# Kernel optimization log

Measured on AMD Instinct MI355X. Metric: run time of the kernel, lower is better.

The kernel has to match this reference:

```python
import jax, jax.numpy as jnp
import numpy as np

B, L, D, H, P, NL, TOPK = 2, 512, 512, 16, 128, 2, 3
DH = D // H
FF = 4 * D
EPS = 1e-5
NEG = -1e9


def _ln(h):
    mu = jnp.mean(h, axis=-1, keepdims=True)
    var = jnp.mean((h - mu) ** 2, axis=-1, keepdims=True)
    return (h - mu) * jax.lax.rsqrt(var + EPS)


def setup_inputs() -> dict:
    key = jax.random.key(0)
    ks = jax.random.split(key, 16)
    def nrm(k, shape, s=0.02):
        return jax.random.normal(k, shape, dtype=jnp.float32) * s
    lengths = jax.random.randint(ks[0], (B,), L // 2, L + 1)
    padding_mask = jnp.arange(L)[None, :] >= lengths[:, None]  # [B,L] bool, True = pad
    return {
        'x': jax.random.normal(ks[1], (L, B, D), dtype=jnp.float32),
        'pos': jax.random.normal(ks[2], (B, L, 3), dtype=jnp.float32),
        'time_emb': jax.random.normal(ks[3], (B, 1, D), dtype=jnp.float32),
        'pair_feat': jax.random.normal(ks[4], (B, L, L, P), dtype=jnp.float32),
        'pos_emb_w': nrm(ks[5], (D, 3), 0.1),
        'pfb_w': nrm(ks[6], (H, P), 0.1),
        'p2n_w1': nrm(ks[7], (P, P)),
        'p2n_w2': nrm(ks[8], (D, P)),
        'adaln_w': nrm(ks[9], (NL, 6 * D, D)),
        'adaln_b': jnp.zeros((NL, 6 * D), jnp.float32),
        'qkv_w': nrm(ks[10], (NL, 3 * D, D)),
        'qkv_b': jnp.zeros((NL, 3 * D), jnp.float32),
        'proj_w': nrm(ks[11], (NL, D, D)),
        'proj_b': jnp.zeros((NL, D), jnp.float32),
        'mlp_w1': nrm(ks[12], (NL, FF, D)),
        'mlp_b1': jnp.zeros((NL, FF), jnp.float32),
        'mlp_w2': nrm(ks[13], (NL, D, FF)),
        'mlp_b2': jnp.zeros((NL, D), jnp.float32),
        'padding_mask': padding_mask,
    }


def _forward(x, pos, time_emb, pair_feat, pos_emb_w, pfb_w, p2n_w1, p2n_w2,
             adaln_w, adaln_b, qkv_w, qkv_b, proj_w, proj_b,
             mlp_w1, mlp_b1, mlp_w2, mlp_b2, padding_mask):
    x = jnp.swapaxes(x, 0, 1)  # [B,L,D]
    keep = (~padding_mask).astype(x.dtype)  # [B,L]
    pos_embedding = (pos @ pos_emb_w.T) * keep[..., None]  # [B,L,D], masked_fill(pad,0)
    # pair bias: SiLU -> Linear(P,H), then permute to [B,H,L,L]
    pfb = jnp.einsum('blmp,hp->bhlm', jax.nn.silu(pair_feat), pfb_w)
    # mask pair features on both residue axes
    pf = pair_feat * keep[:, None, :, None] * keep[:, :, None, None]  # [B,L,L,P]
    # topk over dim=1 (rows) per (b, col): transpose so rows are last axis
    col_scores = jnp.swapaxes(jnp.mean(pfb, axis=1), 1, 2)  # [B, L(col), L(row)]
    _, idx = jax.lax.top_k(col_scores, TOPK)  # [B, L, K]
    idx = jnp.moveaxis(idx, 2, 1)  # [B, K, L]
    f2n = jnp.mean(jnp.take_along_axis(pf, idx[..., None], axis=1), axis=1)  # [B,L,P]
    f2n = jax.nn.silu(f2n @ p2n_w1.T) @ p2n_w2.T  # pair2node MLP -> [B,L,D]
    x = x + f2n  # condition stream
    cond = jax.nn.silu(x)
    scale = 1.0 / np.sqrt(DH)
    h = pos_embedding
    for l in range(NL):  # DiT blocks (adaLN modulation from cond, MHA with pair bias, GELU MLP)
        hin = h + time_emb
        mod = cond @ adaln_w[l].T + adaln_b[l]  # [B,L,6D]
        sh_a, sc_a, g_a, sh_m, sc_m, g_m = jnp.split(mod, 6, axis=-1)
        a = _ln(hin) * (1.0 + sc_a) + sh_a
        q, k, v = jnp.split(a @ qkv_w[l].T + qkv_b[l], 3, axis=-1)
        q = q.reshape(B, L, H, DH)
        k = k.reshape(B, L, H, DH)
        v = v.reshape(B, L, H, DH)
        s = jnp.einsum('blhd,bmhd->bhlm', q, k) * scale + pfb
        s = jnp.where(padding_mask[:, None, None, :], NEG, s)
        o = jnp.einsum('bhlm,bmhd->blhd', jax.nn.softmax(s, axis=-1), v).reshape(B, L, D)
        hin = hin + g_a * (o @ proj_w[l].T + proj_b[l])
        m = _ln(hin) * (1.0 + sc_m) + sh_m
        m = jax.nn.gelu(m @ mlp_w1[l].T + mlp_b1[l]) @ mlp_w2[l].T + mlp_b2[l]
        h = hin + g_m * m
    return h  # [B,L,D]


def reference(x, pos, time_emb, pair_feat, pos_emb_w, pfb_w, p2n_w1, p2n_w2,
              adaln_w, adaln_b, qkv_w, qkv_b, proj_w, proj_b,
              mlp_w1, mlp_b1, mlp_w2, mlp_b2, padding_mask):
    return _forward(x, pos, time_emb, pair_feat, pos_emb_w, pfb_w, p2n_w1, p2n_w2,
                    adaln_w, adaln_b, qkv_w, qkv_b, proj_w, proj_b,
                    mlp_w1, mlp_b1, mlp_w2, mlp_b2, padding_mask)
```

## Files before the change

kernel.cpp:

```cpp
#include <hip/hip_runtime.h>
#include <hip/hip_bf16.h>
#include <math.h>

#define B_  2
#define L_  512
#define D_  512
#define H_  16
#define P_  128
#define NL_ 2
#define DH_ 32
#define FF_ 2048
#define NT_ (B_*L_)

typedef __bf16 bf16_t;
typedef bf16_t bf16x8 __attribute__((ext_vector_type(8)));
typedef bf16_t bf16x4 __attribute__((ext_vector_type(4)));
typedef bf16_t bf16x2 __attribute__((ext_vector_type(2)));
typedef float  f32x4  __attribute__((ext_vector_type(4)));

__device__ __forceinline__ float siluf(float x){ return x / (1.f + __expf(-x)); }
__device__ __forceinline__ float geluf(float x){
  const float c = 0.7978845608028654f;
  float x3 = x*x*x;
  return 0.5f*x*(1.f + tanhf(c*(x + 0.044715f*x3)));
}

__device__ __forceinline__ void gload16(const bf16_t* g, bf16_t* l){
  __builtin_amdgcn_global_load_lds(
      (const __attribute__((address_space(1))) unsigned int*)g,
      (__attribute__((address_space(3))) unsigned int*)l, 16, 0, 0);
}

__global__ __launch_bounds__(256) void k_cvtw(const float* __restrict__ s0,
      const float* __restrict__ s1, const float* __restrict__ s2,
      const float* __restrict__ s3, const float* __restrict__ s4,
      bf16_t* __restrict__ dst){
  const size_t c0=3145728, c1=4718592, c2=5242880, c3=7340032, c4=9437184;
  size_t e = ((size_t)blockIdx.x*256 + threadIdx.x)*4;
  if (e >= c4) return;
  const float* s; size_t off;
  if      (e < c0){ s=s0; off=e; }
  else if (e < c1){ s=s1; off=e-c0; }
  else if (e < c2){ s=s2; off=e-c1; }
  else if (e < c3){ s=s3; off=e-c2; }
  else            { s=s4; off=e-c3; }
  float4 v = *(const float4*)(s + off);
  bf16x4 o; o[0]=(bf16_t)v.x; o[1]=(bf16_t)v.y; o[2]=(bf16_t)v.z; o[3]=(bf16_t)v.w;
  *(bf16x4*)(dst + e) = o;
}

__global__ __launch_bounds__(256) void k_posemb(const float* __restrict__ pos,
      const float* __restrict__ w, const int* __restrict__ maskp,
      float* __restrict__ h, float* __restrict__ keepf){
  int n = blockIdx.x;
  float kf = (maskp[n] != 0) ? 0.f : 1.f;
  if (threadIdx.x == 0) keepf[n] = kf;
  float p0 = pos[n*3+0], p1 = pos[n*3+1], p2 = pos[n*3+2];
  for (int d = threadIdx.x; d < D_; d += 256){
    float v = p0*w[d*3+0] + p1*w[d*3+1] + p2*w[d*3+2];
    h[(size_t)n*D_ + d] = kf*v;
  }
}

__global__ __launch_bounds__(256) void k_pfb2(const float* __restrict__ pair,
      const float* __restrict__ w, bf16_t* __restrict__ pfb, float* __restrict__ colm){
  int blk = blockIdx.x;
  int mc = blk & 1;
  int n  = blk >> 1;
  int b = n >> 9, l = n & 511;
  int tid = threadIdx.x;
  __shared__ float sw[16][128];
  {
    float4* swv = (float4*)&sw[0][0];
    const float4* wv = (const float4*)w;
    swv[tid] = wv[tid];
    swv[tid + 256] = wv[tid + 256];
  }
  __syncthreads();
  int m = mc*256 + tid;
  const float* rowp = pair + (((size_t)n)*512 + m)*128;
  float acc[16] = {};
  #pragma unroll 4
  for (int pc = 0; pc < 32; ++pc){
    float4 v = ((const float4*)rowp)[pc];
    v.x = siluf(v.x); v.y = siluf(v.y); v.z = siluf(v.z); v.w = siluf(v.w);
    #pragma unroll
    for (int hh = 0; hh < 16; ++hh){
      float4 wv = *(const float4*)&sw[hh][pc*4];
      acc[hh] += v.x*wv.x + v.y*wv.y + v.z*wv.z + v.w*wv.w;
    }
  }
  float mean = 0.f;
  #pragma unroll
  for (int hh = 0; hh < 16; ++hh) mean += acc[hh];
  colm[((size_t)n)*512 + m] = mean * (1.f/16.f);
  #pragma unroll
  for (int hh = 0; hh < 16; ++hh)
    pfb[(((size_t)(b*16 + hh))*512 + l)*512 + m] = (bf16_t)acc[hh];
}

__global__ __launch_bounds__(128) void k_topk_f2n(const float* __restrict__ colm,
      const float* __restrict__ pair, const float* __restrict__ keepf,
      const float* __restrict__ w1, const float* __restrict__ w2,
      const float* __restrict__ xin, bf16_t* __restrict__ cond){
  int n = blockIdx.x; int b = n >> 9, m = n & 511;
  __shared__ int sidx[3];
  __shared__ float f2n_s[128];
  __shared__ float u_s[128];
  int tid = threadIdx.x;
  if (tid < 64){
    const float* colbase = colm + ((size_t)b*512)*512 + m;
    float v[8];
    #pragma unroll
    for (int i = 0; i < 8; ++i) v[i] = colbase[(size_t)(tid + 64*i)*512];
    int c0 = -1, c1 = -1;
    for (int r = 0; r < 3; ++r){
      float bv = -INFINITY; int bi = 1 << 30;
      #pragma unroll
      for (int i = 0; i < 8; ++i){
        int idx = tid + 64*i;
        bool excl = (idx == c0) || (idx == c1);
        float val = v[i];
        if (!excl && (val > bv || (val == bv && idx < bi))){ bv = val; bi = idx; }
      }
      for (int o = 32; o > 0; o >>= 1){
        float ov = __shfl_down(bv, o);
        int   oi = __shfl_down(bi, o);
        if (ov > bv || (ov == bv && oi < bi)){ bv = ov; bi = oi; }
      }
      bi = __shfl(bi, 0);
      if (tid == 0) sidx[r] = bi;
      if (r == 0) c0 = bi; else c1 = bi;
    }
  }
  __syncthreads();
  int i0 = sidx[0], i1 = sidx[1], i2 = sidx[2];
  float kc = keepf[n];
  float k0 = keepf[b*512 + i0], k1 = keepf[b*512 + i1], k2 = keepf[b*512 + i2];
  {
    int p = tid;
    float s = k0*pair[(((size_t)(b*512 + i0))*512 + m)*128 + p]
            + k1*pair[(((size_t)(b*512 + i1))*512 + m)*128 + p]
            + k2*pair[(((size_t)(b*512 + i2))*512 + m)*128 + p];
    f2n_s[p] = s * kc * (1.f/3.f);
  }
  __syncthreads();
  {
    int j = tid;
    const float* wr = w1 + (size_t)j*128;
    float acc = 0.f;
    #pragma unroll 8
    for (int p = 0; p < 128; ++p) acc += f2n_s[p]*wr[p];
    u_s[j] = siluf(acc);
  }
  __syncthreads();
  for (int d = tid; d < 512; d += 128){
    const float* wr = w2 + (size_t)d*128;
    float acc = 0.f;
    #pragma unroll 8
    for (int p = 0; p < 128; ++p) acc += u_s[p]*wr[p];
    float xv = xin[((size_t)(m*2 + b))*512 + d];
    cond[(size_t)n*512 + d] = (bf16_t)siluf(xv + acc);
  }
}

__global__ __launch_bounds__(128) void k_lnmod2(const float* __restrict__ hbase,
      const float* __restrict__ te, const float* __restrict__ mod,
      bf16_t* __restrict__ out, int sh_off, int sc_off){
  int n = blockIdx.x; int b = n >> 9;
  int tid = threadIdx.x;
  float4 v = ((const float4*)(hbase + (size_t)n*512))[tid];
  if (te){
    float4 t = ((const float4*)(te + (size_t)b*512))[tid];
    v.x += t.x; v.y += t.y; v.z += t.z; v.w += t.w;
  }
  float s = v.x + v.y + v.z + v.w;
  float q = v.x*v.x + v.y*v.y + v.z*v.z + v.w*v.w;
  #pragma unroll
  for (int o = 1; o < 64; o <<= 1){ s += __shfl_xor(s, o); q += __shfl_xor(q, o); }
  __shared__ float s2[2], q2[2];
  if ((tid & 63) == 0){ s2[tid >> 6] = s; q2[tid >> 6] = q; }
  __syncthreads();
  float S = s2[0] + s2[1], Q = q2[0] + q2[1];
  float mean = S * (1.f/512.f);
  float var  = Q * (1.f/512.f) - mean*mean;
  float rstd = rsqrtf(var + 1e-5f);
  const float* mrow = mod + (size_t)n*3072;
  float4 sc = *(const float4*)(mrow + sc_off + tid*4);
  float4 sh = *(const float4*)(mrow + sh_off + tid*4);
  bf16x4 rv;
  rv[0] = (bf16_t)((v.x - mean)*rstd*(1.f + sc.x) + sh.x);
  rv[1] = (bf16_t)((v.y - mean)*rstd*(1.f + sc.y) + sh.y);
  rv[2] = (bf16_t)((v.z - mean)*rstd*(1.f + sc.z) + sh.z);
  rv[3] = (bf16_t)((v.w - mean)*rstd*(1.f + sc.w) + sh.w);
  *(bf16x4*)(out + (size_t)n*512 + tid*4) = rv;
}

template<bool SMALL>
__global__ __launch_bounds__(256) void k_gemm_bf(const bf16_t* __restrict__ A,
      const bf16_t* __restrict__ Bw, const float* __restrict__ bias,
      int M, int N, int K, int epi,
      float* __restrict__ outf, bf16_t* __restrict__ outb,
      const float* __restrict__ res, const float* __restrict__ gate,
      const float* __restrict__ te, bf16_t* __restrict__ vT){
  const int BN = SMALL ? 32 : 64;
  __shared__ __align__(16) bf16_t As[64*64];
  __shared__ __align__(16) bf16_t Bs[(SMALL?32:64)*64];
  int tid = threadIdx.x;
  int m0 = blockIdx.y*64, n0 = blockIdx.x*BN;
  int lane = tid & 63, wid = tid >> 6;
  int wr = SMALL ? wid : (wid>>1);
  int wc = SMALL ? 0 : (wid&1);
  const int FM = SMALL ? 1 : 2;
  const int WMR = SMALL ? 16 : 32;
  int frow = lane & 15, g = lane >> 4;
  f32x4 acc[2][2] = {};
  for (int k0 = 0; k0 < K; k0 += 64){
    {
      int e = tid;
      #pragma unroll
      for (int i = 0; i < 2; ++i, e += 256){
        int row = e >> 3, cb = e & 7;
        gload16(A + (size_t)(m0+row)*K + k0 + ((cb ^ (row&7))<<3), As + e*8);
      }
      e = tid;
      #pragma unroll
      for (int i = 0; i < (SMALL?1:2); ++i, e += 256){
        int row = e >> 3, cb = e & 7;
        gload16(Bw + (size_t)(n0+row)*K + k0 + ((cb ^ (row&7))<<3), Bs + e*8);
      }
    }
    __syncthreads();
    #pragma unroll
    for (int ks = 0; ks < 2; ++ks){
      bf16x8 af[2], bfv[2];
      #pragma unroll
      for (int fm = 0; fm < FM; ++fm){
        int ar = wr*WMR + fm*16 + frow;
        af[fm] = *(const bf16x8*)&As[ar*64 + (((ks*4+g) ^ (ar&7))<<3)];
      }
      #pragma unroll
      for (int fn = 0; fn < 2; ++fn){
        int br = wc*32 + fn*16 + frow;
        bfv[fn] = *(const bf16x8*)&Bs[br*64 + (((ks*4+g) ^ (br&7))<<3)];
      }
      #pragma unroll
      for (int fm = 0; fm < FM; ++fm)
        #pragma unroll
        for (int fn = 0; fn < 2; ++fn)
          acc[fm][fn] = __builtin_amdgcn_mfma_f32_16x16x32_bf16(af[fm], bfv[fn], acc[fm][fn], 0,0,0);
    }
    __syncthreads();
  }
  #pragma unroll
  for (int fm = 0; fm < FM; ++fm){
    #pragma unroll
    for (int fn = 0; fn < 2; ++fn){
      int n = n0 + wc*32 + fn*16 + frow;
      float bb = bias[n];
      int row0 = m0 + wr*WMR + fm*16 + g*4;
      if (epi == 3 && n >= 1024){
        int hh = (n-1024)>>5, dh = (n-1024)&31;
        int b = row0>>9, ll = row0&511;
        bf16x4 pv;
        #pragma unroll
        for (int i = 0; i < 4; ++i){
          float v = acc[fm][fn][i] + bb;
          outb[(size_t)(row0+i)*N + n] = (bf16_t)v;
          pv[i] = (bf16_t)v;
        }
        *(bf16x4*)&vT[(((size_t)(b*16+hh))*32 + dh)*512 + ll] = pv;
      } else {
        #pragma unroll
        for (int i = 0; i < 4; ++i){
          int row = row0 + i;
          float v = acc[fm][fn][i] + bb;
          if (epi == 1){
            v = res[(size_t)row*N + n] + te[(row>>9)*D_ + n] + gate[(size_t)row*(6*D_) + n]*v;
            outf[(size_t)row*N + n] = v;
          } else if (epi == 2){
            outb[(size_t)row*N + n] = (bf16_t)geluf(v);
          } else if (epi == 3){
            outb[(size_t)row*N + n] = (bf16_t)v;
          } else if (epi == 4){
            v = res[(size_t)row*N + n] + gate[(size_t)row*(6*D_) + n]*v;
            outf[(size_t)row*N + n] = v;
          } else {
            outf[(size_t)row*N + n] = v;
          }
        }
      }
    }
  }
}

__global__ __launch_bounds__(256) void k_attn2(const bf16_t* __restrict__ qkv,
      const bf16_t* __restrict__ vT, const bf16_t* __restrict__ pfb,
      const float* __restrict__ keepf, bf16_t* __restrict__ obuf){
  __shared__ float ss[16][516];
  __shared__ float opart[4][16][33];
  __shared__ float inv_s[16];
  int blk = blockIdx.x;
  int qt = blk & 31;
  int bh = blk >> 5;
  int b = bh >> 4, h = bh & 15;
  int r0 = qt*16;
  int tid = threadIdx.x;
  int lane = tid & 63, w = tid >> 6;
  int frow = lane & 15, g = lane >> 4;
  const float scale = 0.17677669529663687f;
  bf16x8 qf = *(const bf16x8*)(qkv + (size_t)(b*512 + r0 + frow)*1536 + h*32 + g*8);
  for (int t = 0; t < 8; ++t){
    int kc = w*128 + t*16;
    bf16x8 kf = *(const bf16x8*)(qkv + (size_t)(b*512 + kc + frow)*1536 + 512 + h*32 + g*8);
    f32x4 s4 = {};
    s4 = __builtin_amdgcn_mfma_f32_16x16x32_bf16(qf, kf, s4, 0,0,0);
    int tok = kc + frow;
    float kp = keepf[b*512 + tok];
    const bf16_t* pf = pfb + ((size_t)bh*512 + r0 + g*4)*512 + tok;
    #pragma unroll
    for (int i = 0; i < 4; ++i){
      float sv = s4[i]*scale + (float)pf[(size_t)i*512];
      sv = (kp == 0.f) ? -1e9f : sv;
      ss[g*4+i][tok] = sv;
    }
  }
  __syncthreads();
  {
    int r = tid >> 4, mo = tid & 15;
    float mx = -INFINITY;
    #pragma unroll 8
    for (int t2 = 0; t2 < 32; ++t2) mx = fmaxf(mx, ss[r][mo + 16*t2]);
    #pragma unroll
    for (int o = 1; o < 16; o <<= 1) mx = fmaxf(mx, __shfl_xor(mx, o));
    float sum = 0.f;
    #pragma unroll 8
    for (int t2 = 0; t2 < 32; ++t2){
      int m = mo + 16*t2;
      float e = __expf(ss[r][m] - mx);
      ss[r][m] = e;
      sum += e;
    }
    #pragma unroll
    for (int o = 1; o < 16; o <<= 1) sum += __shfl_xor(sum, o);
    if (mo == 0) inv_s[r] = 1.f/sum;
  }
  __syncthreads();
  f32x4 oacc[2] = {};
  for (int t = 0; t < 4; ++t){
    int kc = w*128 + t*32;
    float4 p0 = *(const float4*)&ss[frow][kc + g*8];
    float4 p1 = *(const float4*)&ss[frow][kc + g*8 + 4];
    bf16x8 pfr;
    pfr[0]=(bf16_t)p0.x; pfr[1]=(bf16_t)p0.y; pfr[2]=(bf16_t)p0.z; pfr[3]=(bf16_t)p0.w;
    pfr[4]=(bf16_t)p1.x; pfr[5]=(bf16_t)p1.y; pfr[6]=(bf16_t)p1.z; pfr[7]=(bf16_t)p1.w;
    #pragma unroll
    for (int fn = 0; fn < 2; ++fn){
      bf16x8 vf = *(const bf16x8*)(vT + ((size_t)bh*32 + fn*16 + frow)*512 + kc + g*8);
      oacc[fn] = __builtin_amdgcn_mfma_f32_16x16x32_bf16(pfr, vf, oacc[fn], 0,0,0);
    }
  }
  #pragma unroll
  for (int fn = 0; fn < 2; ++fn)
    #pragma unroll
    for (int i = 0; i < 4; ++i)
      opart[w][g*4+i][fn*16+frow] = oacc[fn][i];
  __syncthreads();
  {
    int q = tid >> 4, dh = (tid & 15)*2;
    float o0 = 0.f, o1 = 0.f;
    #pragma unroll
    for (int ww = 0; ww < 4; ++ww){ o0 += opart[ww][q][dh]; o1 += opart[ww][q][dh+1]; }
    float inv = inv_s[q];
    bf16x2 ov; ov[0] = (bf16_t)(o0*inv); ov[1] = (bf16_t)(o1*inv);
    *(bf16x2*)(obuf + (size_t)(b*512 + r0 + q)*512 + h*32 + dh) = ov;
  }
}

extern "C" void kernel_launch(void* const* d_in, const int* in_sizes, int n_in,
                              void* d_out, int out_size, void* d_ws, size_t ws_size,
                              hipStream_t stream){
  (void)in_sizes; (void)n_in; (void)out_size; (void)ws_size;
  const float* x        = (const float*)d_in[0];
  const float* pos      = (const float*)d_in[1];
  const float* time_emb = (const float*)d_in[2];
  const float* pair     = (const float*)d_in[3];
  const float* pos_w    = (const float*)d_in[4];
  const float* pfb_w    = (const float*)d_in[5];
  const float* p2n_w1   = (const float*)d_in[6];
  const float* p2n_w2   = (const float*)d_in[7];
  const float* adaln_w  = (const float*)d_in[8];
  const float* adaln_b  = (const float*)d_in[9];
  const float* qkv_w    = (const float*)d_in[10];
  const float* qkv_b    = (const float*)d_in[11];
  const float* proj_w   = (const float*)d_in[12];
  const float* proj_b   = (const float*)d_in[13];
  const float* mlp_w1   = (const float*)d_in[14];
  const float* mlp_b1   = (const float*)d_in[15];
  const float* mlp_w2   = (const float*)d_in[16];
  const float* mlp_b2   = (const float*)d_in[17];
  const int*   maskp    = (const int*)d_in[18];

  float* W = (float*)d_ws;
  size_t off = 0;
  auto alloc = [&](size_t nfw){ float* p = W + off; off += nfw; return p; };
  float*  h     = alloc(524288);
  float*  hin2  = alloc(524288);
  float*  modb  = alloc(3145728);
  float*  colm  = alloc(524288);
  float*  keepf = alloc(1024);
  bf16_t* pfbb  = (bf16_t*)alloc(4194304);
  bf16_t* condb = (bf16_t*)alloc(262144);
  bf16_t* abuf  = (bf16_t*)alloc(262144);
  bf16_t* qkvb  = (bf16_t*)alloc(786432);
  bf16_t* vTb   = (bf16_t*)alloc(262144);
  bf16_t* midb  = (bf16_t*)alloc(1048576);
  bf16_t* obuf  = (bf16_t*)alloc(262144);
  bf16_t* wB    = (bf16_t*)alloc(4718592);
  bf16_t* wA  = wB;
  bf16_t* wQ  = wB + 3145728;
  bf16_t* wP  = wB + 4718592;
  bf16_t* wM1 = wB + 5242880;
  bf16_t* wM2 = wB + 7340032;

  k_cvtw<<<9216, 256, 0, stream>>>(adaln_w, qkv_w, proj_w, mlp_w1, mlp_w2, wB);
  k_posemb<<<NT_, 256, 0, stream>>>(pos, pos_w, maskp, h, keepf);
  k_pfb2<<<NT_*2, 256, 0, stream>>>(pair, pfb_w, pfbb, colm);
  k_topk_f2n<<<NT_, 128, 0, stream>>>(colm, pair, keepf, p2n_w1, p2n_w2, x, condb);

  for (int l = 0; l < NL_; ++l){
    k_gemm_bf<false><<<dim3(48,16), 256, 0, stream>>>(condb, wA + (size_t)l*3072*512,
        adaln_b + (size_t)l*3072, NT_, 3072, 512, 0, modb, nullptr, nullptr, nullptr, nullptr, nullptr);
    k_lnmod2<<<NT_, 128, 0, stream>>>(h, time_emb, modb, abuf, 0, D_);
    k_gemm_bf<false><<<dim3(24,16), 256, 0, stream>>>(abuf, wQ + (size_t)l*1536*512,
        qkv_b + (size_t)l*1536, NT_, 1536, 512, 3, nullptr, qkvb, nullptr, nullptr, nullptr, vTb);
    k_attn2<<<B_*H_*32, 256, 0, stream>>>(qkvb, vTb, pfbb, keepf, obuf);
    k_gemm_bf<true><<<dim3(16,16), 256, 0, stream>>>(obuf, wP + (size_t)l*512*512,
        proj_b + (size_t)l*512, NT_, 512, 512, 1, hin2, nullptr, h, modb + 2*D_, time_emb, nullptr);
    k_lnmod2<<<NT_, 128, 0, stream>>>(hin2, nullptr, modb, abuf, 3*D_, 4*D_);
    k_gemm_bf<false><<<dim3(32,16), 256, 0, stream>>>(abuf, wM1 + (size_t)l*2048*512,
        mlp_b1 + (size_t)l*2048, NT_, 2048, 512, 2, nullptr, midb, nullptr, nullptr, nullptr, nullptr);
    float* hout = (l == NL_-1) ? (float*)d_out : h;
    k_gemm_bf<true><<<dim3(16,16), 256, 0, stream>>>(midb, wM2 + (size_t)l*512*2048,
        mlp_b2 + (size_t)l*512, NT_, 512, 2048, 4, hout, nullptr, hin2, modb + 5*D_, nullptr, nullptr);
  }
}
```

Baseline: 346.8 us.

## Merge preprocessing kernels, batch both adaLN GEMMs, double-buffer GEMM LDS tiles

Three preprocessing kernels (weight conversion, position embedding, pair bias) become one launch that dispatches on block index. The two per-layer adaLN modulation GEMMs become a single N=6144 GEMM before the layer loop, since both consume the same cond input and adaln_w is contiguous across layers. Downstream kernels take a row stride for the wider mod buffer. The bf16 GEMM also gains double-buffered LDS staging so the next K tile loads while the current one computes, at the cost of twice the shared memory per block.

Measured after the change: 332.7 us. 1.04x faster.

```diff
diff --git a/kernel.cpp b/kernel.cpp
--- a/kernel.cpp
+++ b/kernel.cpp
@@ -31,48 +31,52 @@
       (__attribute__((address_space(3))) unsigned int*)l, 16, 0, 0);
 }
 
-__global__ __launch_bounds__(256) void k_cvtw(const float* __restrict__ s0,
-      const float* __restrict__ s1, const float* __restrict__ s2,
-      const float* __restrict__ s3, const float* __restrict__ s4,
-      bf16_t* __restrict__ dst){
-  const size_t c0=3145728, c1=4718592, c2=5242880, c3=7340032, c4=9437184;
-  size_t e = ((size_t)blockIdx.x*256 + threadIdx.x)*4;
-  if (e >= c4) return;
-  const float* s; size_t off;
-  if      (e < c0){ s=s0; off=e; }
-  else if (e < c1){ s=s1; off=e-c0; }
-  else if (e < c2){ s=s2; off=e-c1; }
-  else if (e < c3){ s=s3; off=e-c2; }
-  else            { s=s4; off=e-c3; }
-  float4 v = *(const float4*)(s + off);
-  bf16x4 o; o[0]=(bf16_t)v.x; o[1]=(bf16_t)v.y; o[2]=(bf16_t)v.z; o[3]=(bf16_t)v.w;
-  *(bf16x4*)(dst + e) = o;
-}
-
-__global__ __launch_bounds__(256) void k_posemb(const float* __restrict__ pos,
-      const float* __restrict__ w, const int* __restrict__ maskp,
-      float* __restrict__ h, float* __restrict__ keepf){
-  int n = blockIdx.x;
-  float kf = (maskp[n] != 0) ? 0.f : 1.f;
-  if (threadIdx.x == 0) keepf[n] = kf;
-  float p0 = pos[n*3+0], p1 = pos[n*3+1], p2 = pos[n*3+2];
-  for (int d = threadIdx.x; d < D_; d += 256){
-    float v = p0*w[d*3+0] + p1*w[d*3+1] + p2*w[d*3+2];
-    h[(size_t)n*D_ + d] = kf*v;
-  }
-}
-
-__global__ __launch_bounds__(256) void k_pfb2(const float* __restrict__ pair,
-      const float* __restrict__ w, bf16_t* __restrict__ pfb, float* __restrict__ colm){
-  int blk = blockIdx.x;
+#define NB_CVT 9216
+#define NB_POS 1024
+__global__ __launch_bounds__(256) void k_pre(
+      const float* __restrict__ s0, const float* __restrict__ s1,
+      const float* __restrict__ s2, const float* __restrict__ s3,
+      const float* __restrict__ s4, bf16_t* __restrict__ wdst,
+      const float* __restrict__ pos, const float* __restrict__ posw,
+      const int* __restrict__ maskp, float* __restrict__ h, float* __restrict__ keepf,
+      const float* __restrict__ pair, const float* __restrict__ pfw,
+      bf16_t* __restrict__ pfb, float* __restrict__ colm){
+  __shared__ float sw[16][128];
+  int bid = blockIdx.x;
+  int tid = threadIdx.x;
+  if (bid < NB_CVT){
+    const size_t c0=3145728, c1=4718592, c2=5242880, c3=7340032, c4=9437184;
+    size_t e = ((size_t)bid*256 + tid)*4;
+    if (e >= c4) return;
+    const float* s; size_t off;
+    if      (e < c0){ s=s0; off=e; }
+    else if (e < c1){ s=s1; off=e-c0; }
+    else if (e < c2){ s=s2; off=e-c1; }
+    else if (e < c3){ s=s3; off=e-c2; }
+    else            { s=s4; off=e-c3; }
+    float4 v = *(const float4*)(s + off);
+    bf16x4 o; o[0]=(bf16_t)v.x; o[1]=(bf16_t)v.y; o[2]=(bf16_t)v.z; o[3]=(bf16_t)v.w;
+    *(bf16x4*)(wdst + e) = o;
+    return;
+  }
+  if (bid < NB_CVT + NB_POS){
+    int n = bid - NB_CVT;
+    float kf = (maskp[n] != 0) ? 0.f : 1.f;
+    if (tid == 0) keepf[n] = kf;
+    float p0 = pos[n*3+0], p1 = pos[n*3+1], p2 = pos[n*3+2];
+    for (int d = tid; d < D_; d += 256){
+      float v = p0*posw[d*3+0] + p1*posw[d*3+1] + p2*posw[d*3+2];
+      h[(size_t)n*D_ + d] = kf*v;
+    }
+    return;
+  }
+  int blk = bid - NB_CVT - NB_POS;
   int mc = blk & 1;
   int n  = blk >> 1;
   int b = n >> 9, l = n & 511;
-  int tid = threadIdx.x;
-  __shared__ float sw[16][128];
   {
     float4* swv = (float4*)&sw[0][0];
-    const float4* wv = (const float4*)w;
+    const float4* wv = (const float4*)pfw;
     swv[tid] = wv[tid];
     swv[tid + 256] = wv[tid + 256];
   }
@@ -166,7 +170,7 @@
 
 __global__ __launch_bounds__(128) void k_lnmod2(const float* __restrict__ hbase,
       const float* __restrict__ te, const float* __restrict__ mod,
-      bf16_t* __restrict__ out, int sh_off, int sc_off){
+      bf16_t* __restrict__ out, int sh_off, int sc_off, int mstride){
   int n = blockIdx.x; int b = n >> 9;
   int tid = threadIdx.x;
   float4 v = ((const float4*)(hbase + (size_t)n*512))[tid];
@@ -185,7 +189,7 @@
   float mean = S * (1.f/512.f);
   float var  = Q * (1.f/512.f) - mean*mean;
   float rstd = rsqrtf(var + 1e-5f);
-  const float* mrow = mod + (size_t)n*3072;
+  const float* mrow = mod + (size_t)n*mstride;
   float4 sc = *(const float4*)(mrow + sc_off + tid*4);
   float4 sh = *(const float4*)(mrow + sh_off + tid*4);
   bf16x4 rv;
@@ -201,11 +205,11 @@
       const bf16_t* __restrict__ Bw, const float* __restrict__ bias,
       int M, int N, int K, int epi,
       float* __restrict__ outf, bf16_t* __restrict__ outb,
-      const float* __restrict__ res, const float* __restrict__ gate,
+      const float* __restrict__ res, const float* __restrict__ gate, int gate_ld,
       const float* __restrict__ te, bf16_t* __restrict__ vT){
   const int BN = SMALL ? 32 : 64;
-  __shared__ __align__(16) bf16_t As[64*64];
-  __shared__ __align__(16) bf16_t Bs[(SMALL?32:64)*64];
+  __shared__ __align__(16) bf16_t As[2][64*64];
+  __shared__ __align__(16) bf16_t Bs[2][(SMALL?32:64)*64];
   int tid = threadIdx.x;
   int m0 = blockIdx.y*64, n0 = blockIdx.x*BN;
   int lane = tid & 63, wid = tid >> 6;
@@ -215,34 +219,34 @@
   const int WMR = SMALL ? 16 : 32;
   int frow = lane & 15, g = lane >> 4;
   f32x4 acc[2][2] = {};
-  for (int k0 = 0; k0 < K; k0 += 64){
-    {
-      int e = tid;
-      #pragma unroll
-      for (int i = 0; i < 2; ++i, e += 256){
-        int row = e >> 3, cb = e & 7;
-        gload16(A + (size_t)(m0+row)*K + k0 + ((cb ^ (row&7))<<3), As + e*8);
-      }
-      e = tid;
-      #pragma unroll
-      for (int i = 0; i < (SMALL?1:2); ++i, e += 256){
-        int row = e >> 3, cb = e & 7;
-        gload16(Bw + (size_t)(n0+row)*K + k0 + ((cb ^ (row&7))<<3), Bs + e*8);
-      }
-    }
-    __syncthreads();
+
+  auto stage = [&](int buf, int k0){
+    int e = tid;
+    #pragma unroll
+    for (int i = 0; i < 2; ++i, e += 256){
+      int row = e >> 3, cb = e & 7;
+      gload16(A + (size_t)(m0+row)*K + k0 + ((cb ^ (row&7))<<3), &As[buf][e*8]);
+    }
+    e = tid;
+    #pragma unroll
+    for (int i = 0; i < (SMALL?1:2); ++i, e += 256){
+      int row = e >> 3, cb = e & 7;
+      gload16(Bw + (size_t)(n0+row)*K + k0 + ((cb ^ (row&7))<<3), &Bs[buf][e*8]);
+    }
+  };
+  auto compute = [&](int buf){
     #pragma unroll
     for (int ks = 0; ks < 2; ++ks){
       bf16x8 af[2], bfv[2];
       #pragma unroll
       for (int fm = 0; fm < FM; ++fm){
         int ar = wr*WMR + fm*16 + frow;
-        af[fm] = *(const bf16x8*)&As[ar*64 + (((ks*4+g) ^ (ar&7))<<3)];
+        af[fm] = *(const bf16x8*)&As[buf][ar*64 + (((ks*4+g) ^ (ar&7))<<3)];
       }
       #pragma unroll
       for (int fn = 0; fn < 2; ++fn){
         int br = wc*32 + fn*16 + frow;
-        bfv[fn] = *(const bf16x8*)&Bs[br*64 + (((ks*4+g) ^ (br&7))<<3)];
+        bfv[fn] = *(const bf16x8*)&Bs[buf][br*64 + (((ks*4+g) ^ (br&7))<<3)];
       }
       #pragma unroll
       for (int fm = 0; fm < FM; ++fm)
@@ -250,8 +254,19 @@
         for (int fn = 0; fn < 2; ++fn)
           acc[fm][fn] = __builtin_amdgcn_mfma_f32_16x16x32_bf16(af[fm], bfv[fn], acc[fm][fn], 0,0,0);
     }
+  };
+
+  stage(0, 0);
+  __syncthreads();
+  int cur = 0;
+  for (int k0 = 64; k0 < K; k0 += 64){
+    stage(cur^1, k0);
+    compute(cur);
     __syncthreads();
-  }
+    cur ^= 1;
+  }
+  compute(cur);
+
   #pragma unroll
   for (int fm = 0; fm < FM; ++fm){
     #pragma unroll
@@ -276,14 +291,14 @@
           int row = row0 + i;
           float v = acc[fm][fn][i] + bb;
           if (epi == 1){
-            v = res[(size_t)row*N + n] + te[(row>>9)*D_ + n] + gate[(size_t)row*(6*D_) + n]*v;
+            v = res[(size_t)row*N + n] + te[(row>>9)*D_ + n] + gate[(size_t)row*gate_ld + n]*v;
             outf[(size_t)row*N + n] = v;
           } else if (epi == 2){
             outb[(size_t)row*N + n] = (bf16_t)geluf(v);
           } else if (epi == 3){
             outb[(size_t)row*N + n] = (bf16_t)v;
           } else if (epi == 4){
-            v = res[(size_t)row*N + n] + gate[(size_t)row*(6*D_) + n]*v;
+            v = res[(size_t)row*N + n] + gate[(size_t)row*gate_ld + n]*v;
             outf[(size_t)row*N + n] = v;
           } else {
             outf[(size_t)row*N + n] = v;
@@ -406,7 +421,7 @@
   auto alloc = [&](size_t nfw){ float* p = W + off; off += nfw; return p; };
   float*  h     = alloc(524288);
   float*  hin2  = alloc(524288);
-  float*  modb  = alloc(3145728);
+  float*  modb  = alloc(6291456);
   float*  colm  = alloc(524288);
   float*  keepf = alloc(1024);
   bf16_t* pfbb  = (bf16_t*)alloc(4194304);
@@ -423,25 +438,29 @@
   bf16_t* wM1 = wB + 5242880;
   bf16_t* wM2 = wB + 7340032;
 
-  k_cvtw<<<9216, 256, 0, stream>>>(adaln_w, qkv_w, proj_w, mlp_w1, mlp_w2, wB);
-  k_posemb<<<NT_, 256, 0, stream>>>(pos, pos_w, maskp, h, keepf);
-  k_pfb2<<<NT_*2, 256, 0, stream>>>(pair, pfb_w, pfbb, colm);
+  k_pre<<<NB_CVT + NB_POS + NT_*2, 256, 0, stream>>>(
+      adaln_w, qkv_w, proj_w, mlp_w1, mlp_w2, wB,
+      pos, pos_w, maskp, h, keepf,
+      pair, pfb_w, pfbb, colm);
   k_topk_f2n<<<NT_, 128, 0, stream>>>(colm, pair, keepf, p2n_w1, p2n_w2, x, condb);
+  k_gemm_bf<false><<<dim3(96,16), 256, 0, stream>>>(condb, wA, adaln_b,
+      NT_, 6144, 512, 0, modb, nullptr, nullptr, nullptr, 0, nullptr, nullptr);
 
   for (int l = 0; l < NL_; ++l){
-    k_gemm_bf<false><<<dim3(48,16), 256, 0, stream>>>(condb, wA + (size_t)l*3072*512,
-        adaln_b + (size_t)l*3072, NT_, 3072, 512, 0, modb, nullptr, nullptr, nullptr, nullptr, nullptr);
-    k_lnmod2<<<NT_, 128, 0, stream>>>(h, time_emb, modb, abuf, 0, D_);
+    const float* modl = modb + (size_t)l*3072;
+    k_lnmod2<<<NT_, 128, 0, stream>>>(h, time_emb, modl, abuf, 0, 512, 6144);
     k_gemm_bf<false><<<dim3(24,16), 256, 0, stream>>>(abuf, wQ + (size_t)l*1536*512,
-        qkv_b + (size_t)l*1536, NT_, 1536, 512, 3, nullptr, qkvb, nullptr, nullptr, nullptr, vTb);
+        qkv_b + (size_t)l*1536, NT_, 1536, 512, 3, nullptr, qkvb, nullptr, nullptr, 0, nullptr, vTb);
     k_attn2<<<B_*H_*32, 256, 0, stream>>>(qkvb, vTb, pfbb, keepf, obuf);
     k_gemm_bf<true><<<dim3(16,16), 256, 0, stream>>>(obuf, wP + (size_t)l*512*512,
-        proj_b + (size_t)l*512, NT_, 512, 512, 1, hin2, nullptr, h, modb + 2*D_, time_emb, nullptr);
-    k_lnmod2<<<NT_, 128, 0, stream>>>(hin2, nullptr, modb, abuf, 3*D_, 4*D_);
+        proj_b + (size_t)l*512, NT_, 512, 512, 1, hin2, nullptr, h,
+        (const float*)(modl + 2*512), 6144, time_emb, nullptr);
+    k_lnmod2<<<NT_, 128, 0, stream>>>(hin2, nullptr, modl, abuf, 3*512, 4*512, 6144);
     k_gemm_bf<false><<<dim3(32,16), 256, 0, stream>>>(abuf, wM1 + (size_t)l*2048*512,
-        mlp_b1 + (size_t)l*2048, NT_, 2048, 512, 2, nullptr, midb, nullptr, nullptr, nullptr, nullptr);
+        mlp_b1 + (size_t)l*2048, NT_, 2048, 512, 2, nullptr, midb, nullptr, nullptr, 0, nullptr, nullptr);
     float* hout = (l == NL_-1) ? (float*)d_out : h;
     k_gemm_bf<true><<<dim3(16,16), 256, 0, stream>>>(midb, wM2 + (size_t)l*512*2048,
-        mlp_b2 + (size_t)l*512, NT_, 512, 2048, 4, hout, nullptr, hin2, modb + 5*D_, nullptr, nullptr);
-  }
-}
+        mlp_b2 + (size_t)l*512, NT_, 512, 2048, 4, hout, nullptr, hin2,
+        (const float*)(modl + 5*512), 6144, nullptr, nullptr);
+  }
+}
```
